# Kernel optimization log

Measured on AMD Instinct MI355X. Metric: run time of the kernel, lower is better.

## Reference

```python
import jax, jax.numpy as jnp
import numpy as np

B, S, E = 4, 2048, 1024
H = 16
D = E // H  # head dim = 64
ROPE_BASE = 10000.0


def _rope(t):
    # t: [B, H, S, D]; rotate-half RoPE (YaRN with scale=1 reduces to this)
    half = D // 2
    inv_freq = 1.0 / (ROPE_BASE ** (jnp.arange(0, half, dtype=jnp.float32) / half))
    pos = jnp.arange(t.shape[2], dtype=jnp.float32)
    ang = pos[:, None] * inv_freq[None, :]          # [S, D/2]
    cos, sin = jnp.cos(ang), jnp.sin(ang)
    t1, t2 = t[..., :half], t[..., half:]
    return jnp.concatenate([t1 * cos - t2 * sin, t1 * sin + t2 * cos], axis=-1)


def setup_inputs() -> dict:
    key = jax.random.key(0)
    ks = jax.random.split(key, 6)
    sc = 1.0 / np.sqrt(E)
    return {
        "x": jax.random.normal(ks[0], (B, S, E), jnp.float32),
        "Wq": jax.random.normal(ks[1], (E, E), jnp.float32) * sc,
        "Wk": jax.random.normal(ks[2], (E, E), jnp.float32) * sc,
        "Wv": jax.random.normal(ks[3], (E, E), jnp.float32) * sc,
        "Wp": jax.random.normal(ks[4], (E, E), jnp.float32) * sc,
        "bp": jnp.zeros((E,), jnp.float32),
    }


def reference(x, Wq, Wk, Wv, Wp, bp):
    seq = x.shape[1]
    def heads(W):
        # project then split heads -> [B, H, S, D]
        return (x @ W.T).reshape(B, seq, H, D).transpose(0, 2, 1, 3)
    q = _rope(heads(Wq))
    k = _rope(heads(Wk))
    v = heads(Wv)
    score = jnp.einsum("bhqd,bhkd->bhqk", q, k) * (D ** -0.5)
    mask = jnp.tril(jnp.ones((seq, seq), dtype=bool))
    score = jnp.where(mask[None, None], score, -jnp.inf)
    attn = jax.nn.softmax(score, axis=-1)
    out = jnp.einsum("bhqk,bhkd->bhqd", attn, v)
    out = out.transpose(0, 2, 1, 3).reshape(B, seq, E)
    return out @ Wp.T + bp  # dropout is identity at inference
```

## Files before the change

### kernel.cpp

```cpp
#include <hip/hip_runtime.h>
#include <hip/hip_bf16.h>

typedef __hip_bfloat16 bf16;
typedef __attribute__((ext_vector_type(8))) short bf16x8;
typedef __attribute__((ext_vector_type(4))) short bf16x4;
typedef __attribute__((ext_vector_type(4))) float f32x4;

static constexpr int B_ = 4, S_ = 2048, E_ = 1024, H_ = 16, D_ = 64;
static constexpr int M_ = B_ * S_;
static constexpr int NQKV = 3 * E_;

__device__ __forceinline__ void gload_lds16(const void* g, void* l) {
  __builtin_amdgcn_global_load_lds(
      (const __attribute__((address_space(1))) unsigned int*)g,
      (__attribute__((address_space(3))) unsigned int*)l, 16, 0, 0);
}

__global__ void cast_kernel(const float* __restrict__ src, bf16* __restrict__ dst, int n8) {
  int t = blockIdx.x * blockDim.x + threadIdx.x;
  if (t >= n8) return;
  float4 a = ((const float4*)src)[2 * t];
  float4 b = ((const float4*)src)[2 * t + 1];
  union { bf16x8 v; bf16 e[8]; } u;
  u.e[0] = __float2bfloat16(a.x); u.e[1] = __float2bfloat16(a.y);
  u.e[2] = __float2bfloat16(a.z); u.e[3] = __float2bfloat16(a.w);
  u.e[4] = __float2bfloat16(b.x); u.e[5] = __float2bfloat16(b.y);
  u.e[6] = __float2bfloat16(b.z); u.e[7] = __float2bfloat16(b.w);
  ((bf16x8*)dst)[t] = u.v;
}

__global__ void rope_table_kernel(float* __restrict__ cost, float* __restrict__ sint) {
  int t = blockIdx.x * blockDim.x + threadIdx.x;
  if (t >= S_ * 32) return;
  int i = t & 31, s = t >> 5;
  float inv_freq = powf(10000.0f, -(float)i / 32.0f);
  float ang = (float)s * inv_freq;
  cost[t] = cosf(ang);
  sint[t] = sinf(ang);
}

template <int OUTMODE>
__launch_bounds__(256)
__global__ void gemm_bt_kernel(const bf16* __restrict__ A, int lda,
                               const bf16* __restrict__ Bw, int ldb,
                               void* __restrict__ Cv, int ldc,
                               const float* __restrict__ bias,
                               int K, int ntiles_n,
                               const float* __restrict__ cost,
                               const float* __restrict__ sint,
                               bf16* __restrict__ qh,
                               bf16* __restrict__ khsw,
                               bf16* __restrict__ vtsw) {
  __shared__ bf16 Asm[128 * 32];
  __shared__ bf16 Bsm[128 * 32];
  int t = threadIdx.x;
  int lane = t & 63, w = t >> 6;
  int wr = w >> 1, wc = w & 1;
  int l15 = lane & 15, l4 = lane >> 4;
  int n0 = (blockIdx.x % ntiles_n) * 128;
  int m0 = (blockIdx.x / ntiles_n) * 128;

  f32x4 acc[4][4];
#pragma unroll
  for (int i = 0; i < 4; i++)
#pragma unroll
    for (int j = 0; j < 4; j++) acc[i][j] = (f32x4){0.f, 0.f, 0.f, 0.f};

  for (int k0 = 0; k0 < K; k0 += 32) {
#pragma unroll
    for (int i = 0; i < 2; i++) {
      int c = i * 256 + t;
      int row = c >> 2, kg = c & 3;
      const bf16* ga = A + (size_t)(m0 + row) * lda + k0 + kg * 8;
      gload_lds16(ga, &Asm[(i * 256 + w * 64) * 8]);
      const bf16* gb = Bw + (size_t)(n0 + row) * ldb + k0 + kg * 8;
      gload_lds16(gb, &Bsm[(i * 256 + w * 64) * 8]);
    }
    __syncthreads();
    bf16x8 am[4], bn[4];
#pragma unroll
    for (int i = 0; i < 4; i++) {
      am[i] = *(const bf16x8*)&Asm[(wr * 64 + i * 16 + l15) * 32 + l4 * 8];
      bn[i] = *(const bf16x8*)&Bsm[(wc * 64 + i * 16 + l15) * 32 + l4 * 8];
    }
#pragma unroll
    for (int i = 0; i < 4; i++)
#pragma unroll
      for (int j = 0; j < 4; j++)
        acc[i][j] = __builtin_amdgcn_mfma_f32_16x16x32_bf16(am[i], bn[j], acc[i][j], 0, 0, 0);
    __syncthreads();
  }

  if (OUTMODE == 1) {
#pragma unroll
    for (int i = 0; i < 4; i++)
#pragma unroll
      for (int j = 0; j < 4; j++)
#pragma unroll
        for (int r = 0; r < 4; r++) {
          int m = m0 + wr * 64 + i * 16 + l4 * 4 + r;
          int n = n0 + wc * 64 + j * 16 + l15;
          ((float*)Cv)[(size_t)m * ldc + n] = acc[i][j][r] + bias[n];
        }
  } else {
    int btype = n0 >> 10;
    int h = ((n0 & 1023) >> 6) + wc;
    if (btype < 2) {
      const float qsc = (btype == 0) ? 0.18033688011112043f : 1.0f;
#pragma unroll
      for (int i = 0; i < 4; i++) {
        int mbase = m0 + wr * 64 + i * 16 + l4 * 4;
#pragma unroll
        for (int r = 0; r < 4; r++) {
          int m = mbase + r;
          int s = m & 2047, b = m >> 11;
#pragma unroll
          for (int j = 0; j < 2; j++) {
            int d1 = j * 16 + l15;
            float c = cost[s * 32 + d1], sn = sint[s * 32 + d1];
            float t1 = acc[i][j][r], t2 = acc[i][j + 2][r];
            bf16 o1 = __float2bfloat16((t1 * c - t2 * sn) * qsc);
            bf16 o2 = __float2bfloat16((t1 * sn + t2 * c) * qsc);
            if (btype == 0) {
              bf16* dst = qh + ((size_t)(b * H_ + h) * S_ + s) * D_;
              dst[d1] = o1;
              dst[d1 + 32] = o2;
            } else {
              int row = s & 63, kt = s >> 6, sz = (row & 7) * 8;
              bf16* dst = khsw + (((size_t)(b * H_ + h) * 32 + kt) * 64 + row) * 64;
              dst[d1 ^ sz] = o1;
              dst[(d1 + 32) ^ sz] = o2;
            }
          }
        }
      }
    } else {
#pragma unroll
      for (int i = 0; i < 4; i++) {
        int mbase = m0 + wr * 64 + i * 16 + l4 * 4;
        int c0 = mbase & 63, kt = (mbase >> 6) & 31, b = mbase >> 11;
#pragma unroll
        for (int j = 0; j < 4; j++) {
          int d = j * 16 + l15;
          union { bf16x4 v; short e[4]; } pk;
#pragma unroll
          for (int r = 0; r < 4; r++) {
            bf16 tv = __float2bfloat16(acc[i][j][r]);
            pk.e[r] = *(short*)&tv;
          }
          *(bf16x4*)&vtsw[(((size_t)(b * H_ + h) * 32 + kt) * 64 + d) * 64 +
                          (c0 ^ ((d & 7) * 8))] = pk.v;
        }
      }
    }
  }
}

__launch_bounds__(256, 3)
__global__ void attn_kernel(const bf16* __restrict__ qh, const bf16* __restrict__ khsw,
                            const bf16* __restrict__ vtsw, bf16* __restrict__ attn) {
  __shared__ bf16 Ksm[2][4096];
  __shared__ bf16 Vsm[2][4096];
  __shared__ bf16 Plds[4][2][16][72];
  int t = threadIdx.x, lane = t & 63, w = t >> 6;
  int l15 = lane & 15, l4 = lane >> 4;
  int swz = (l15 & 7) * 8;
  int st = 15 - (blockIdx.x >> 6);
  int bh = blockIdx.x & 63;
  int b = bh >> 4, h = bh & 15;
  const bf16* Qh = qh + (size_t)bh * S_ * D_;

#define STAGE(bb, kt)                                                          \
  do {                                                                         \
    const bf16* kb_ = khsw + ((size_t)bh * 32 + (kt)) * 4096 + w * 1024 + lane * 8; \
    const bf16* vb_ = vtsw + ((size_t)bh * 32 + (kt)) * 4096 + w * 1024 + lane * 8; \
    gload_lds16(kb_, &Ksm[bb][w * 1024]);                                      \
    gload_lds16(kb_ + 512, &Ksm[bb][w * 1024 + 512]);                          \
    gload_lds16(vb_, &Vsm[bb][w * 1024]);                                      \
    gload_lds16(vb_ + 512, &Vsm[bb][w * 1024 + 512]);                          \
  } while (0)

  int q0 = st * 128 + w * 32;
  int nt = 2 * st + 2;

  bf16x8 qf[2][2];
#pragma unroll
  for (int qg = 0; qg < 2; qg++)
#pragma unroll
    for (int sl = 0; sl < 2; sl++)
      qf[qg][sl] = *(const bf16x8*)&Qh[(size_t)(q0 + qg * 16 + l15) * D_ + sl * 32 + l4 * 8];

  f32x4 acc_o[2][4];
  float lsum[2] = {0.f, 0.f};
#pragma unroll
  for (int qg = 0; qg < 2; qg++)
#pragma unroll
    for (int j = 0; j < 4; j++) acc_o[qg][j] = (f32x4){0.f, 0.f, 0.f, 0.f};

  STAGE(0, 0);
  __syncthreads();
  int buf = 0;
  for (int ti = 0; ti < nt; ti++) {
    int kb = ti * 64;
    if (ti + 1 < nt) STAGE(buf ^ 1, ti + 1);
    if (kb <= q0 + 31) {
      bool maskt = (kb + 63 > q0);
      f32x4 s[2][4];
#pragma unroll
      for (int cb = 0; cb < 4; cb++) {
        bf16x8 kf0 = *(const bf16x8*)&Ksm[buf][(cb * 16 + l15) * 64 + ((l4 * 8) ^ swz)];
        bf16x8 kf1 = *(const bf16x8*)&Ksm[buf][(cb * 16 + l15) * 64 + ((32 + l4 * 8) ^ swz)];
#pragma unroll
        for (int qg = 0; qg < 2; qg++) {
          f32x4 z = (f32x4){0.f, 0.f, 0.f, 0.f};
          z = __builtin_amdgcn_mfma_f32_16x16x32_bf16(kf0, qf[qg][0], z, 0, 0, 0);
          z = __builtin_amdgcn_mfma_f32_16x16x32_bf16(kf1, qf[qg][1], z, 0, 0, 0);
          s[qg][cb] = z;
        }
      }
#pragma unroll
      for (int qg = 0; qg < 2; qg++) {
        int q = q0 + qg * 16 + l15;
#pragma unroll
        for (int cb = 0; cb < 4; cb++) {
          union { bf16x4 v; short e[4]; } pk;
#pragma unroll
          for (int r = 0; r < 4; r++) {
            float p = exp2f(s[qg][cb][r]);
            if (maskt && (kb + cb * 16 + l4 * 4 + r > q)) p = 0.f;
            lsum[qg] += p;
            bf16 pb16 = __float2bfloat16(p);
            pk.e[r] = *(short*)&pb16;
          }
          *(bf16x4*)&Plds[w][qg][l15][cb * 16 + l4 * 4] = pk.v;
        }
      }
#pragma unroll
      for (int qg = 0; qg < 2; qg++) {
        bf16x8 pf0 = *(const bf16x8*)&Plds[w][qg][l15][l4 * 8];
        bf16x8 pf1 = *(const bf16x8*)&Plds[w][qg][l15][32 + l4 * 8];
#pragma unroll
        for (int db = 0; db < 4; db++) {
          bf16x8 vf0 = *(const bf16x8*)&Vsm[buf][(db * 16 + l15) * 64 + ((l4 * 8) ^ swz)];
          bf16x8 vf1 = *(const bf16x8*)&Vsm[buf][(db * 16 + l15) * 64 + ((32 + l4 * 8) ^ swz)];
          acc_o[qg][db] = __builtin_amdgcn_mfma_f32_16x16x32_bf16(pf0, vf0, acc_o[qg][db], 0, 0, 0);
          acc_o[qg][db] = __builtin_amdgcn_mfma_f32_16x16x32_bf16(pf1, vf1, acc_o[qg][db], 0, 0, 0);
        }
      }
    }
    __syncthreads();
    buf ^= 1;
  }

  float invr[2][4];
#pragma unroll
  for (int qg = 0; qg < 2; qg++) {
    float ls = lsum[qg];
    ls += __shfl_xor(ls, 16, 64);
    ls += __shfl_xor(ls, 32, 64);
    float inv = 1.0f / ls;
#pragma unroll
    for (int r = 0; r < 4; r++) invr[qg][r] = __shfl(inv, l4 * 4 + r, 64);
  }

#pragma unroll
  for (int qg = 0; qg < 2; qg++)
#pragma unroll
    for (int db = 0; db < 4; db++)
#pragma unroll
      for (int r = 0; r < 4; r++) {
        int qa = q0 + qg * 16 + l4 * 4 + r;
        attn[(size_t)(b * S_ + qa) * E_ + h * 64 + db * 16 + l15] =
            __float2bfloat16(acc_o[qg][db][r] * invr[qg][r]);
      }
#undef STAGE
}

extern "C" void kernel_launch(void* const* d_in, const int* in_sizes, int n_in,
                              void* d_out, int out_size, void* d_ws, size_t ws_size,
                              hipStream_t stream) {
  const float* x  = (const float*)d_in[0];
  const float* Wq = (const float*)d_in[1];
  const float* Wk = (const float*)d_in[2];
  const float* Wv = (const float*)d_in[3];
  const float* Wp = (const float*)d_in[4];
  const float* bp = (const float*)d_in[5];

  char* ws = (char*)d_ws;
  bf16* x_bf = (bf16*)(ws + 0);
  bf16* w_bf = (bf16*)(ws + 16777216);
  bf16* aout = (bf16*)(ws + 25165824);
  bf16* qh   = (bf16*)(ws + 75497472);
  bf16* khsw = (bf16*)(ws + 92274688);
  bf16* vtsw = (bf16*)(ws + 109051904);
  float* cost = (float*)(ws + 125829120);
  float* sint = (float*)(ws + 126091264);

  cast_kernel<<<4096, 256, 0, stream>>>(x, x_bf, M_ * E_ / 8);
  cast_kernel<<<512, 256, 0, stream>>>(Wq, w_bf + 0 * E_ * E_, E_ * E_ / 8);
  cast_kernel<<<512, 256, 0, stream>>>(Wk, w_bf + 1 * E_ * E_, E_ * E_ / 8);
  cast_kernel<<<512, 256, 0, stream>>>(Wv, w_bf + 2 * E_ * E_, E_ * E_ / 8);
  cast_kernel<<<512, 256, 0, stream>>>(Wp, w_bf + 3 * E_ * E_, E_ * E_ / 8);
  rope_table_kernel<<<256, 256, 0, stream>>>(cost, sint);

  gemm_bt_kernel<2><<<(M_ / 128) * (NQKV / 128), 256, 0, stream>>>(
      x_bf, E_, w_bf, E_, nullptr, 0, nullptr, E_, NQKV / 128,
      cost, sint, qh, khsw, vtsw);

  attn_kernel<<<16 * 64, 256, 0, stream>>>(qh, khsw, vtsw, aout);

  gemm_bt_kernel<1><<<(M_ / 128) * (E_ / 128), 256, 0, stream>>>(
      aout, E_, w_bf + 3 * E_ * E_, E_, d_out, E_, bp, E_, E_ / 128,
      nullptr, nullptr, nullptr, nullptr, nullptr);
}
```

Measured before the change: 199.9 us.

## Fuse prep kernels, deepen GEMM K-tile with swizzled LDS, add MFMA priority hints

Merges the five cast launches and the RoPE table launch into one prep kernel, and folds the Q scale into an interleaved cos/sin float2 table. The GEMM K-step doubles from 32 to 64 with an XOR-swizzled LDS layout, halving barriers per K and aiming to avoid bank conflicts. The attention kernel raises wave priority around its MFMA sections with s_setprio. Together these target launch overhead, barrier and LDS-conflict stalls, and scheduling, at the cost of twice the GEMM shared memory, which may lower occupancy.

```diff
diff --git a/kernel.cpp b/kernel.cpp
--- a/kernel.cpp
+++ b/kernel.cpp
@@ -16,9 +16,8 @@
       (__attribute__((address_space(3))) unsigned int*)l, 16, 0, 0);
 }
 
-__global__ void cast_kernel(const float* __restrict__ src, bf16* __restrict__ dst, int n8) {
-  int t = blockIdx.x * blockDim.x + threadIdx.x;
-  if (t >= n8) return;
+__device__ __forceinline__ void cast8(const float* __restrict__ src,
+                                      bf16* __restrict__ dst, int t) {
   float4 a = ((const float4*)src)[2 * t];
   float4 b = ((const float4*)src)[2 * t + 1];
   union { bf16x8 v; bf16 e[8]; } u;
@@ -29,14 +28,28 @@
   ((bf16x8*)dst)[t] = u.v;
 }
 
-__global__ void rope_table_kernel(float* __restrict__ cost, float* __restrict__ sint) {
-  int t = blockIdx.x * blockDim.x + threadIdx.x;
-  if (t >= S_ * 32) return;
-  int i = t & 31, s = t >> 5;
-  float inv_freq = powf(10000.0f, -(float)i / 32.0f);
-  float ang = (float)s * inv_freq;
-  cost[t] = cosf(ang);
-  sint[t] = sinf(ang);
+__global__ void prep_kernel(const float* __restrict__ x, const float* __restrict__ Wq,
+                            const float* __restrict__ Wk, const float* __restrict__ Wv,
+                            const float* __restrict__ Wp,
+                            bf16* __restrict__ x_bf, bf16* __restrict__ w_bf,
+                            float2* __restrict__ qtab, float2* __restrict__ ktab) {
+  int bid = blockIdx.x;
+  if (bid < 4096) {
+    cast8(x, x_bf, bid * 256 + threadIdx.x);
+  } else if (bid < 6144) {
+    int wi = (bid - 4096) >> 9;
+    const float* src = wi == 0 ? Wq : wi == 1 ? Wk : wi == 2 ? Wv : Wp;
+    cast8(src, w_bf + (size_t)wi * E_ * E_, ((bid - 4096) & 511) * 256 + threadIdx.x);
+  } else {
+    int tt = (bid - 6144) * 256 + threadIdx.x;
+    int i = tt & 31, s = tt >> 5;
+    float inv_freq = powf(10000.0f, -(float)i / 32.0f);
+    float ang = (float)s * inv_freq;
+    float c = cosf(ang), sn = sinf(ang);
+    const float qsc = 0.18033688011112043f;
+    qtab[tt] = make_float2(c * qsc, sn * qsc);
+    ktab[tt] = make_float2(c, sn);
+  }
 }
 
 template <int OUTMODE>
@@ -46,13 +59,13 @@
                                void* __restrict__ Cv, int ldc,
                                const float* __restrict__ bias,
                                int K, int ntiles_n,
-                               const float* __restrict__ cost,
-                               const float* __restrict__ sint,
+                               const float2* __restrict__ qtab,
+                               const float2* __restrict__ ktab,
                                bf16* __restrict__ qh,
                                bf16* __restrict__ khsw,
                                bf16* __restrict__ vtsw) {
-  __shared__ bf16 Asm[128 * 32];
-  __shared__ bf16 Bsm[128 * 32];
+  __shared__ bf16 Asm[128 * 64];
+  __shared__ bf16 Bsm[128 * 64];
   int t = threadIdx.x;
   int lane = t & 63, w = t >> 6;
   int wr = w >> 1, wc = w & 1;
@@ -66,28 +79,34 @@
 #pragma unroll
     for (int j = 0; j < 4; j++) acc[i][j] = (f32x4){0.f, 0.f, 0.f, 0.f};
 
-  for (int k0 = 0; k0 < K; k0 += 32) {
-#pragma unroll
-    for (int i = 0; i < 2; i++) {
-      int c = i * 256 + t;
-      int row = c >> 2, kg = c & 3;
-      const bf16* ga = A + (size_t)(m0 + row) * lda + k0 + kg * 8;
-      gload_lds16(ga, &Asm[(i * 256 + w * 64) * 8]);
-      const bf16* gb = Bw + (size_t)(n0 + row) * ldb + k0 + kg * 8;
-      gload_lds16(gb, &Bsm[(i * 256 + w * 64) * 8]);
+  for (int k0 = 0; k0 < K; k0 += 64) {
+#pragma unroll
+    for (int p = 0; p < 4; p++) {
+      int c = p * 256 + t;
+      int row = c >> 3, kg = c & 7;
+      int kgs = kg ^ (row & 7);
+      const bf16* ga = A + (size_t)(m0 + row) * lda + k0 + kgs * 8;
+      gload_lds16(ga, &Asm[(p * 256 + w * 64) * 8]);
+      const bf16* gb = Bw + (size_t)(n0 + row) * ldb + k0 + kgs * 8;
+      gload_lds16(gb, &Bsm[(p * 256 + w * 64) * 8]);
     }
     __syncthreads();
-    bf16x8 am[4], bn[4];
-#pragma unroll
-    for (int i = 0; i < 4; i++) {
-      am[i] = *(const bf16x8*)&Asm[(wr * 64 + i * 16 + l15) * 32 + l4 * 8];
-      bn[i] = *(const bf16x8*)&Bsm[(wc * 64 + i * 16 + l15) * 32 + l4 * 8];
+#pragma unroll
+    for (int kk = 0; kk < 2; kk++) {
+      bf16x8 am[4], bn[4];
+#pragma unroll
+      for (int i = 0; i < 4; i++) {
+        int ra = wr * 64 + i * 16 + l15;
+        am[i] = *(const bf16x8*)&Asm[ra * 64 + ((kk * 32 + l4 * 8) ^ ((ra & 7) * 8))];
+        int rb = wc * 64 + i * 16 + l15;
+        bn[i] = *(const bf16x8*)&Bsm[rb * 64 + ((kk * 32 + l4 * 8) ^ ((rb & 7) * 8))];
+      }
+#pragma unroll
+      for (int i = 0; i < 4; i++)
+#pragma unroll
+        for (int j = 0; j < 4; j++)
+          acc[i][j] = __builtin_amdgcn_mfma_f32_16x16x32_bf16(am[i], bn[j], acc[i][j], 0, 0, 0);
     }
-#pragma unroll
-    for (int i = 0; i < 4; i++)
-#pragma unroll
-      for (int j = 0; j < 4; j++)
-        acc[i][j] = __builtin_amdgcn_mfma_f32_16x16x32_bf16(am[i], bn[j], acc[i][j], 0, 0, 0);
     __syncthreads();
   }
 
@@ -106,7 +125,7 @@
     int btype = n0 >> 10;
     int h = ((n0 & 1023) >> 6) + wc;
     if (btype < 2) {
-      const float qsc = (btype == 0) ? 0.18033688011112043f : 1.0f;
+      const float2* tab = (btype == 0) ? qtab : ktab;
 #pragma unroll
       for (int i = 0; i < 4; i++) {
         int mbase = m0 + wr * 64 + i * 16 + l4 * 4;
@@ -117,10 +136,10 @@
 #pragma unroll
           for (int j = 0; j < 2; j++) {
             int d1 = j * 16 + l15;
-            float c = cost[s * 32 + d1], sn = sint[s * 32 + d1];
+            float2 cs = tab[s * 32 + d1];
             float t1 = acc[i][j][r], t2 = acc[i][j + 2][r];
-            bf16 o1 = __float2bfloat16((t1 * c - t2 * sn) * qsc);
-            bf16 o2 = __float2bfloat16((t1 * sn + t2 * c) * qsc);
+            bf16 o1 = __float2bfloat16(t1 * cs.x - t2 * cs.y);
+            bf16 o2 = __float2bfloat16(t1 * cs.y + t2 * cs.x);
             if (btype == 0) {
               bf16* dst = qh + ((size_t)(b * H_ + h) * S_ + s) * D_;
               dst[d1] = o1;
@@ -206,6 +225,7 @@
     if (kb <= q0 + 31) {
       bool maskt = (kb + 63 > q0);
       f32x4 s[2][4];
+      __builtin_amdgcn_s_setprio(1);
 #pragma unroll
       for (int cb = 0; cb < 4; cb++) {
         bf16x8 kf0 = *(const bf16x8*)&Ksm[buf][(cb * 16 + l15) * 64 + ((l4 * 8) ^ swz)];
@@ -218,6 +238,7 @@
           s[qg][cb] = z;
         }
       }
+      __builtin_amdgcn_s_setprio(0);
 #pragma unroll
       for (int qg = 0; qg < 2; qg++) {
         int q = q0 + qg * 16 + l15;
@@ -235,6 +256,7 @@
           *(bf16x4*)&Plds[w][qg][l15][cb * 16 + l4 * 4] = pk.v;
         }
       }
+      __builtin_amdgcn_s_setprio(1);
 #pragma unroll
       for (int qg = 0; qg < 2; qg++) {
         bf16x8 pf0 = *(const bf16x8*)&Plds[w][qg][l15][l4 * 8];
@@ -247,6 +269,7 @@
           acc_o[qg][db] = __builtin_amdgcn_mfma_f32_16x16x32_bf16(pf1, vf1, acc_o[qg][db], 0, 0, 0);
         }
       }
+      __builtin_amdgcn_s_setprio(0);
     }
     __syncthreads();
     buf ^= 1;
@@ -287,29 +310,24 @@
   const float* bp = (const float*)d_in[5];
 
   char* ws = (char*)d_ws;
-  bf16* x_bf = (bf16*)(ws + 0);
-  bf16* w_bf = (bf16*)(ws + 16777216);
-  bf16* aout = (bf16*)(ws + 25165824);
-  bf16* qh   = (bf16*)(ws + 75497472);
-  bf16* khsw = (bf16*)(ws + 92274688);
-  bf16* vtsw = (bf16*)(ws + 109051904);
-  float* cost = (float*)(ws + 125829120);
-  float* sint = (float*)(ws + 126091264);
-
-  cast_kernel<<<4096, 256, 0, stream>>>(x, x_bf, M_ * E_ / 8);
-  cast_kernel<<<512, 256, 0, stream>>>(Wq, w_bf + 0 * E_ * E_, E_ * E_ / 8);
-  cast_kernel<<<512, 256, 0, stream>>>(Wk, w_bf + 1 * E_ * E_, E_ * E_ / 8);
-  cast_kernel<<<512, 256, 0, stream>>>(Wv, w_bf + 2 * E_ * E_, E_ * E_ / 8);
-  cast_kernel<<<512, 256, 0, stream>>>(Wp, w_bf + 3 * E_ * E_, E_ * E_ / 8);
-  rope_table_kernel<<<256, 256, 0, stream>>>(cost, sint);
+  bf16* x_bf   = (bf16*)(ws + 0);
+  bf16* w_bf   = (bf16*)(ws + (16u << 20));
+  bf16* aout   = (bf16*)(ws + (24u << 20));
+  bf16* qh     = (bf16*)(ws + (40u << 20));
+  bf16* khsw   = (bf16*)(ws + (56u << 20));
+  bf16* vtsw   = (bf16*)(ws + (72u << 20));
+  float2* qtab = (float2*)(ws + (88u << 20));
+  float2* ktab = (float2*)(ws + (88u << 20) + (512u << 10));
+
+  prep_kernel<<<6400, 256, 0, stream>>>(x, Wq, Wk, Wv, Wp, x_bf, w_bf, qtab, ktab);
 
   gemm_bt_kernel<2><<<(M_ / 128) * (NQKV / 128), 256, 0, stream>>>(
       x_bf, E_, w_bf, E_, nullptr, 0, nullptr, E_, NQKV / 128,
-      cost, sint, qh, khsw, vtsw);
+      qtab, ktab, qh, khsw, vtsw);
 
   attn_kernel<<<16 * 64, 256, 0, stream>>>(qh, khsw, vtsw, aout);
 
   gemm_bt_kernel<1><<<(M_ / 128) * (E_ / 128), 256, 0, stream>>>(
-      aout, E_, w_bf + 3 * E_ * E_, E_, d_out, E_, bp, E_, E_ / 128,
+      aout, E_, w_bf + 3 * (size_t)E_ * E_, E_, d_out, E_, bp, E_, E_ / 128,
       nullptr, nullptr, nullptr, nullptr, nullptr);
 }
```

Measured after the change: 176.4 us. 11.7% less time.
